# Optimization experiments

Measured on AMD Instinct MI355X. Metric: run time of the kernel, lower is better.

## Reference

```python
import jax, jax.numpy as jnp
import numpy as np

INPUT_DIM, HIDDEN_DIM, N_HEADS, N_AGENTS = 256, 512, 8, 64
BATCH, N_ENTITIES = 128, 256


def setup_inputs() -> dict:
    key = jax.random.key(0)
    ks = jax.random.split(key, 6)
    x = jax.random.normal(ks[0], (BATCH, N_ENTITIES, INPUT_DIM), dtype=jnp.float32)
    # encode: LeakyReLU -> Linear(input_dim, hidden_dim)
    W_enc = jax.random.normal(ks[1], (INPUT_DIM, HIDDEN_DIM), dtype=jnp.float32) * (1.0 / np.sqrt(INPUT_DIM))
    b_enc = jnp.zeros((HIDDEN_DIM,), dtype=jnp.float32)
    # per-head full hidden x hidden projections, stacked on head axis
    WQ = jax.random.normal(ks[2], (N_HEADS, HIDDEN_DIM, HIDDEN_DIM), dtype=jnp.float32)
    WK = jax.random.normal(ks[3], (N_HEADS, HIDDEN_DIM, HIDDEN_DIM), dtype=jnp.float32)
    WV = jax.random.normal(ks[4], (N_HEADS, HIDDEN_DIM, HIDDEN_DIM), dtype=jnp.float32)
    return {"x": x, "W_enc": W_enc, "b_enc": b_enc, "WQ": WQ, "WK": WK, "WV": WV, "n_agents": N_AGENTS}


def reference(x, W_enc, b_enc, WQ, WK, WV, n_agents):
    scale = 1.0 / np.sqrt(WQ.shape[-1]).astype(np.float32)
    # encode: LeakyReLU(0.01) then Linear
    h = jax.nn.leaky_relu(x, negative_slope=0.01) @ W_enc + b_enc  # [b, e, H]
    ha = h[:, :n_agents]  # [b, a, H]
    # all heads at once: n = head axis
    Q = jnp.einsum('bah,nhd->nbad', ha, WQ)
    K = jnp.einsum('beh,nhd->nbed', h, WK)
    V = jnp.einsum('beh,nhd->nbed', h, WV)
    scores = jnp.einsum('nbad,nbed->nbae', Q, K) * scale
    p = jax.nn.softmax(scores, axis=-1)
    # redundant renormalization from the original code
    prob = p / (jnp.sum(p, axis=-1, keepdims=True) + 1e-12)
    z = jnp.einsum('nbae,nbed->nbad', prob, V)  # [n, b, a, H]
    return jnp.mean(z, axis=0)  # [b, a, H]
```

## Files before the change

kernel.cpp:

```cpp
#include <hip/hip_runtime.h>
#include <math.h>

#define BATCH  128
#define NENT   256
#define INDIM  256
#define HID    512
#define NHEAD  8
#define NAGENT 64
#define SCALE  0.04419417382415922f

typedef unsigned short u16;
typedef unsigned int   u32;

typedef __bf16 bf16x8  __attribute__((ext_vector_type(8)));
typedef float  floatx4 __attribute__((ext_vector_type(4)));
typedef u32    u32x4   __attribute__((ext_vector_type(4)));
typedef u32    u32x2   __attribute__((ext_vector_type(2)));

union Frag {
    u32x4 s;
    struct { u32x2 lo, hi; } p;
    bf16x8 v;
};

__device__ __forceinline__ u16 f2bf(float x) {
    u32 u = __float_as_uint(x);
    return (u16)((u + 0x7FFFu + ((u >> 16) & 1u)) >> 16);
}
__device__ __forceinline__ float bf2f(u16 b) {
    return __uint_as_float(((u32)b) << 16);
}
__device__ __forceinline__ void split4(const float4& r, ushort4& hh, ushort4& hl) {
    hh.x = f2bf(r.x); hl.x = f2bf(r.x - bf2f(hh.x));
    hh.y = f2bf(r.y); hl.y = f2bf(r.y - bf2f(hh.y));
    hh.z = f2bf(r.z); hl.z = f2bf(r.z - bf2f(hh.z));
    hh.w = f2bf(r.w); hl.w = f2bf(r.w - bf2f(hh.w));
}

__global__ __launch_bounds__(256) void wenc_t_kernel(const float* __restrict__ W,
                                                     u16* __restrict__ Wt_h,
                                                     u16* __restrict__ Wt_l) {
    __shared__ float tile[64][68];
    const int bid = blockIdx.x;
    const int k0 = (bid & 3) * 64;
    const int d0 = (bid >> 2) * 64;
    const int t = threadIdx.x;
    const int ki = t >> 2, dc = (t & 3) * 16;
    #pragma unroll
    for (int c = 0; c < 4; ++c)
        *(float4*)&tile[ki][dc + c * 4] =
            *(const float4*)(W + (size_t)(k0 + ki) * HID + d0 + dc + c * 4);
    __syncthreads();
    const int dr = t >> 2, kc = (t & 3) * 16;
    #pragma unroll
    for (int c = 0; c < 4; ++c) {
        float4 v = make_float4(tile[kc + c * 4 + 0][dr], tile[kc + c * 4 + 1][dr],
                               tile[kc + c * 4 + 2][dr], tile[kc + c * 4 + 3][dr]);
        ushort4 hh, hl; split4(v, hh, hl);
        size_t o = (size_t)(d0 + dr) * INDIM + k0 + kc + c * 4;
        *(ushort4*)(Wt_h + o) = hh;
        *(ushort4*)(Wt_l + o) = hl;
    }
}

__global__ __launch_bounds__(256) void enc_kernel(const float* __restrict__ x,
                                                  const u16* __restrict__ Wt_h,
                                                  const u16* __restrict__ Wt_l,
                                                  const float* __restrict__ bias,
                                                  u16* __restrict__ h_h,
                                                  u16* __restrict__ h_l) {
    __shared__ u16 Ah[32][264];
    __shared__ u16 Al[32][264];
    const int r0 = blockIdx.x * 32;
    const int t  = threadIdx.x;
    {
        const int row = t >> 3;
        const float* xr = x + (size_t)(r0 + row) * INDIM;
        #pragma unroll
        for (int j = 0; j < 8; ++j) {
            const int k0 = ((t & 7) + j * 8) * 4;
            float4 v = *(const float4*)(xr + k0);
            v.x = v.x > 0.f ? v.x : 0.01f * v.x;
            v.y = v.y > 0.f ? v.y : 0.01f * v.y;
            v.z = v.z > 0.f ? v.z : 0.01f * v.z;
            v.w = v.w > 0.f ? v.w : 0.01f * v.w;
            ushort4 hh, hl; split4(v, hh, hl);
            *(ushort4*)&Ah[row][k0] = hh;
            *(ushort4*)&Al[row][k0] = hl;
        }
    }
    __syncthreads();

    const int wid = t >> 6, lane = t & 63, l15 = lane & 15, quad = lane >> 4;
    const int mbase = (wid & 1) * 16;
    const int nbase = (wid >> 1) * 256;
    const floatx4 z4 = {0.f, 0.f, 0.f, 0.f};
    floatx4 acc[16];
    #pragma unroll
    for (int i = 0; i < 16; ++i) acc[i] = z4;

    for (int ks = 0; ks < 8; ++ks) {
        const int k = ks * 32 + quad * 8;
        Frag Afh, Afl;
        Afh.s = *(const u32x4*)&Ah[mbase + l15][k];
        Afl.s = *(const u32x4*)&Al[mbase + l15][k];
        #pragma unroll
        for (int nt = 0; nt < 16; ++nt) {
            const int d = nbase + nt * 16 + l15;
            Frag Bh, Bl;
            Bh.s = *(const u32x4*)(Wt_h + (size_t)d * INDIM + k);
            Bl.s = *(const u32x4*)(Wt_l + (size_t)d * INDIM + k);
            floatx4 c = acc[nt];
            c = __builtin_amdgcn_mfma_f32_16x16x32_bf16(Afh.v, Bh.v, c, 0, 0, 0);
            c = __builtin_amdgcn_mfma_f32_16x16x32_bf16(Afh.v, Bl.v, c, 0, 0, 0);
            c = __builtin_amdgcn_mfma_f32_16x16x32_bf16(Afl.v, Bh.v, c, 0, 0, 0);
            acc[nt] = c;
        }
    }
    #pragma unroll
    for (int nt = 0; nt < 16; ++nt) {
        const int d = nbase + nt * 16 + l15;
        const float bv = bias[d];
        #pragma unroll
        for (int r = 0; r < 4; ++r) {
            const float v = acc[nt][r] + bv;
            const u16 hi = f2bf(v);
            const u16 lo = f2bf(v - bf2f(hi));
            const size_t o = (size_t)(r0 + mbase + quad * 4 + r) * HID + d;
            h_h[o] = hi;
            h_l[o] = lo;
        }
    }
}

__global__ __launch_bounds__(256) void ht_kernel(const u16* __restrict__ h_h,
                                                 u16* __restrict__ hT) {
    __shared__ u16 tile[64][72];
    const int bid = blockIdx.x;
    const int dt = bid & 7;
    const int et = (bid >> 3) & 3;
    const int b  = bid >> 5;
    const int t  = threadIdx.x;
    const int r  = t >> 2, cs = (t & 3) * 16;
    const u16* src = h_h + (size_t)(b * 256 + et * 64 + r) * HID + dt * 64 + cs;
    *(ushort4*)&tile[r][cs + 0]  = *(const ushort4*)(src + 0);
    *(ushort4*)&tile[r][cs + 4]  = *(const ushort4*)(src + 4);
    *(ushort4*)&tile[r][cs + 8]  = *(const ushort4*)(src + 8);
    *(ushort4*)&tile[r][cs + 12] = *(const ushort4*)(src + 12);
    __syncthreads();
    const int d = t >> 2, es = (t & 3) * 16;
    u16* dst = hT + (size_t)b * 131072 + (size_t)(dt * 64 + d) * 256 + et * 64 + es;
    #pragma unroll
    for (int c = 0; c < 4; ++c) {
        ushort4 v = make_ushort4(tile[es + c * 4 + 0][d], tile[es + c * 4 + 1][d],
                                 tile[es + c * 4 + 2][d], tile[es + c * 4 + 3][d]);
        *(ushort4*)(dst + c * 4) = v;
    }
}

__global__ __launch_bounds__(256) void wqk_kernel(const float* __restrict__ WQ,
                                                  const float* __restrict__ WK,
                                                  u16* __restrict__ Mt_h,
                                                  u16* __restrict__ Mt_l) {
    __shared__ u16 Ah[64][72], Al[64][72], Bh[64][72], Bl[64][72];
    const int bid = blockIdx.x;
    const int jt = (bid & 7) * 64;
    const int it = ((bid >> 3) & 7) * 64;
    const int n  = bid >> 6;
    const float* qp = WQ + (size_t)n * 262144;
    const float* kp = WK + (size_t)n * 262144;
    const int t = threadIdx.x;
    const int wid = t >> 6, lane = t & 63, l15 = lane & 15, quad = lane >> 4;
    const int srow = t >> 2, sc = (t & 3) * 16;

    const floatx4 z4 = {0.f, 0.f, 0.f, 0.f};
    floatx4 acc[4];
    #pragma unroll
    for (int i = 0; i < 4; ++i) acc[i] = z4;

    for (int kc = 0; kc < HID; kc += 64) {
        #pragma unroll
        for (int f = 0; f < 4; ++f) {
            float4 va = *(const float4*)(kp + (size_t)(jt + srow) * HID + kc + sc + f * 4);
            ushort4 hh, hl; split4(va, hh, hl);
            *(ushort4*)&Ah[srow][sc + f * 4] = hh;
            *(ushort4*)&Al[srow][sc + f * 4] = hl;
            float4 vb = *(const float4*)(qp + (size_t)(it + srow) * HID + kc + sc + f * 4);
            split4(vb, hh, hl);
            *(ushort4*)&Bh[srow][sc + f * 4] = hh;
            *(ushort4*)&Bl[srow][sc + f * 4] = hl;
        }
        __syncthreads();
        #pragma unroll
        for (int ks = 0; ks < 2; ++ks) {
            const int k = ks * 32 + quad * 8;
            Frag Afh, Afl;
            Afh.s = *(const u32x4*)&Ah[wid * 16 + l15][k];
            Afl.s = *(const u32x4*)&Al[wid * 16 + l15][k];
            #pragma unroll
            for (int nt = 0; nt < 4; ++nt) {
                Frag Bfh, Bfl;
                Bfh.s = *(const u32x4*)&Bh[nt * 16 + l15][k];
                Bfl.s = *(const u32x4*)&Bl[nt * 16 + l15][k];
                floatx4 c = acc[nt];
                c = __builtin_amdgcn_mfma_f32_16x16x32_bf16(Afh.v, Bfh.v, c, 0, 0, 0);
                c = __builtin_amdgcn_mfma_f32_16x16x32_bf16(Afh.v, Bfl.v, c, 0, 0, 0);
                c = __builtin_amdgcn_mfma_f32_16x16x32_bf16(Afl.v, Bfh.v, c, 0, 0, 0);
                acc[nt] = c;
            }
        }
        __syncthreads();
    }
    #pragma unroll
    for (int nt = 0; nt < 4; ++nt)
        #pragma unroll
        for (int r = 0; r < 4; ++r) {
            const float v = acc[nt][r] * SCALE;
            const u16 hi = f2bf(v);
            const u16 lo = f2bf(v - bf2f(hi));
            const int j = jt + wid * 16 + quad * 4 + r;
            const int i = it + nt * 16 + l15;
            const size_t o = (size_t)n * 262144 + (size_t)j * HID + i;
            Mt_h[o] = hi;
            Mt_l[o] = lo;
        }
}

__global__ __launch_bounds__(256) void wvt_kernel(const float* __restrict__ WV,
                                                  u16* __restrict__ WVt) {
    __shared__ float tile[64][68];
    const int bid = blockIdx.x;
    const int i0 = (bid & 7) * 64;
    const int o0 = ((bid >> 3) & 7) * 64;
    const int n  = bid >> 6;
    const float* src = WV + (size_t)n * 262144;
    const int t  = threadIdx.x;
    const int di = t >> 2;
    const int dc = (t & 3) * 16;
    #pragma unroll
    for (int c = 0; c < 4; ++c)
        *(float4*)&tile[di][dc + c * 4] =
            *(const float4*)(src + (size_t)(i0 + di) * HID + o0 + dc + c * 4);
    __syncthreads();
    const int dr = t >> 2;
    const int ic = (t & 3) * 16;
    size_t o = (size_t)n * 262144 + (size_t)(o0 + dr) * HID + i0 + ic;
    #pragma unroll
    for (int c = 0; c < 4; ++c) {
        ushort4 v = make_ushort4(f2bf(tile[ic + c * 4 + 0][dr]), f2bf(tile[ic + c * 4 + 1][dr]),
                                 f2bf(tile[ic + c * 4 + 2][dr]), f2bf(tile[ic + c * 4 + 3][dr]));
        *(ushort4*)(WVt + o + c * 4) = v;
    }
}

template<bool USE_HT>
__global__ __launch_bounds__(256, 3) void attn_kernel(const u16* __restrict__ h_h,
                                                      const u16* __restrict__ h_l,
                                                      const u16* __restrict__ Mt_h,
                                                      const u16* __restrict__ Mt_l,
                                                      const u16* __restrict__ WVt,
                                                      const u16* __restrict__ hT,
                                                      float* __restrict__ out) {
    __shared__ __align__(16) char SM[53504];
    u16*   Th  = (u16*)SM;
    u16*   Tl  = (u16*)(SM + 16640);
    float* S   = (float*)SM;
    float* red = (float*)(SM + 33792);
    u16*   HbT = (u16*)SM;
    u16*   U   = (u16*)SM;
    u16*   Pt  = (u16*)(SM + 36864);

    const int bid = blockIdx.x;
    const int x7 = bid & 7;
    const int s  = bid >> 3;
    const int at = s & 1;
    const int n  = (x7 >> 1) | (((s >> 1) & 1) << 2);
    const int b  = ((s >> 2) << 1) | (x7 & 1);

    const int tid  = threadIdx.x;
    const int wid  = tid >> 6;
    const int lane = tid & 63;
    const int l15  = lane & 15;
    const int quad = lane >> 4;

    const u16* Mth = Mt_h + (size_t)n * 262144;
    const u16* Mtl = Mt_l + (size_t)n * 262144;
    const u16* Wv  = WVt  + (size_t)n * 262144;
    const u16* hTb = hT + (size_t)b * 131072;
    const size_t hb_base = (size_t)b * NENT * HID;
    const size_t ha_base = hb_base + (size_t)at * 32 * HID;

    const floatx4 z4 = {0.f, 0.f, 0.f, 0.f};
    floatx4 Sacc[8];
    #pragma unroll
    for (int i = 0; i < 8; ++i) Sacc[i] = z4;

    for (int H = 0; H < 2; ++H) {
        floatx4 Tacc[8];
        #pragma unroll
        for (int i = 0; i < 8; ++i) Tacc[i] = z4;
        Frag Bh[2][4], Bl[2][4];
        auto loadBA = [&](int ksv, Frag* bh, Frag* bl) {
            const int k = ksv * 32 + quad * 8;
            #pragma unroll
            for (int nt = 0; nt < 4; ++nt) {
                const int d = H * 256 + (wid * 4 + nt) * 16 + l15;
                bh[nt].s = *(const u32x4*)(Mth + (size_t)d * HID + k);
                bl[nt].s = *(const u32x4*)(Mtl + (size_t)d * HID + k);
            }
        };
        loadBA(0, Bh[0], Bl[0]);
        #pragma unroll 2
        for (int ks = 0; ks < 16; ++ks) {
            const int cur = ks & 1, nxt = cur ^ 1;
            const int k = ks * 32 + quad * 8;
            Frag Ahf[2], Alf[2];
            #pragma unroll
            for (int mt = 0; mt < 2; ++mt) {
                const size_t ro = ha_base + (size_t)(mt * 16 + l15) * HID + k;
                Ahf[mt].s = *(const u32x4*)(h_h + ro);
                Alf[mt].s = *(const u32x4*)(h_l + ro);
            }
            if (ks < 15) loadBA(ks + 1, Bh[nxt], Bl[nxt]);
            #pragma unroll
            for (int nt = 0; nt < 4; ++nt)
                #pragma unroll
                for (int mt = 0; mt < 2; ++mt) {
                    floatx4 c = Tacc[mt * 4 + nt];
                    c = __builtin_amdgcn_mfma_f32_16x16x32_bf16(Ahf[mt].v, Bh[cur][nt].v, c, 0, 0, 0);
                    c = __builtin_amdgcn_mfma_f32_16x16x32_bf16(Ahf[mt].v, Bl[cur][nt].v, c, 0, 0, 0);
                    c = __builtin_amdgcn_mfma_f32_16x16x32_bf16(Alf[mt].v, Bh[cur][nt].v, c, 0, 0, 0);
                    Tacc[mt * 4 + nt] = c;
                }
        }
        __syncthreads();
        #pragma unroll
        for (int mt = 0; mt < 2; ++mt)
            #pragma unroll
            for (int nt = 0; nt < 4; ++nt)
                #pragma unroll
                for (int r = 0; r < 4; ++r) {
                    const float v = Tacc[mt * 4 + nt][r];
                    const int a  = mt * 16 + quad * 4 + r;
                    const int dl = (wid * 4 + nt) * 16 + l15;
                    const u16 hi = f2bf(v);
                    Th[a * 260 + dl] = hi;
                    Tl[a * 260 + dl] = f2bf(v - bf2f(hi));
                }
        __syncthreads();
        Frag Ahb[2][4], Alb[2][4];
        auto loadAB2 = [&](int ksv, Frag* ah, Frag* al) {
            const int kg = H * 256 + ksv * 32 + quad * 8;
            #pragma unroll
            for (int mt = 0; mt < 4; ++mt) {
                const size_t ro = hb_base + (size_t)((wid * 4 + mt) * 16 + l15) * HID + kg;
                ah[mt].s = *(const u32x4*)(h_h + ro);
                al[mt].s = *(const u32x4*)(h_l + ro);
            }
        };
        loadAB2(0, Ahb[0], Alb[0]);
        #pragma unroll 2
        for (int ks = 0; ks < 8; ++ks) {
            const int cur = ks & 1, nxt = cur ^ 1;
            const int kl = ks * 32 + quad * 8;
            if (ks < 7) loadAB2(ks + 1, Ahb[nxt], Alb[nxt]);
            #pragma unroll
            for (int nt = 0; nt < 2; ++nt) {
                const int ac = nt * 16 + l15;
                Frag Bfh, Bfl;
                Bfh.p.lo = *(const u32x2*)(Th + ac * 260 + kl);
                Bfh.p.hi = *(const u32x2*)(Th + ac * 260 + kl + 4);
                Bfl.p.lo = *(const u32x2*)(Tl + ac * 260 + kl);
                Bfl.p.hi = *(const u32x2*)(Tl + ac * 260 + kl + 4);
                #pragma unroll
                for (int mt = 0; mt < 4; ++mt) {
                    floatx4 c = Sacc[mt * 2 + nt];
                    c = __builtin_amdgcn_mfma_f32_16x16x32_bf16(Ahb[cur][mt].v, Bfh.v, c, 0, 0, 0);
                    c = __builtin_amdgcn_mfma_f32_16x16x32_bf16(Ahb[cur][mt].v, Bfl.v, c, 0, 0, 0);
                    c = __builtin_amdgcn_mfma_f32_16x16x32_bf16(Alb[cur][mt].v, Bfh.v, c, 0, 0, 0);
                    Sacc[mt * 2 + nt] = c;
                }
            }
        }
    }
    __syncthreads();
    #pragma unroll
    for (int mt = 0; mt < 4; ++mt)
        #pragma unroll
        for (int nt = 0; nt < 2; ++nt)
            #pragma unroll
            for (int r = 0; r < 4; ++r) {
                const int e = (wid * 4 + mt) * 16 + quad * 4 + r;
                const int a = nt * 16 + l15;
                S[e * 33 + a] = Sacc[mt * 2 + nt][r];
            }
    __syncthreads();
    {
        const int a   = tid & 31;
        const int seg = tid >> 5;
        float v[32];
        #pragma unroll
        for (int i = 0; i < 32; ++i) v[i] = S[(seg * 32 + i) * 33 + a];
        float mx = v[0];
        #pragma unroll
        for (int i = 1; i < 32; ++i) mx = fmaxf(mx, v[i]);
        red[a * 8 + seg] = mx;
        __syncthreads();
        float gmx = red[a * 8 + 0];
        #pragma unroll
        for (int i = 1; i < 8; ++i) gmx = fmaxf(gmx, red[a * 8 + i]);
        __syncthreads();
        float sum = 0.f;
        #pragma unroll
        for (int i = 0; i < 32; ++i) { v[i] = expf(v[i] - gmx); sum += v[i]; }
        red[a * 8 + seg] = sum;
        __syncthreads();
        float tot = 0.f;
        #pragma unroll
        for (int i = 0; i < 8; ++i) tot += red[a * 8 + i];
        const float inv = 1.0f / tot;
        #pragma unroll
        for (int i = 0; i < 32; ++i)
            Pt[a * 260 + seg * 32 + i] = f2bf(v[i] * inv);
    }
    __syncthreads();
    floatx4 Uacc[16];
    #pragma unroll
    for (int i = 0; i < 16; ++i) Uacc[i] = z4;
    const int d0w = wid * 128;
    if (USE_HT) {
        Frag Bc[2][8];
        auto loadBC = [&](int etv, Frag* bc) {
            #pragma unroll
            for (int dt = 0; dt < 8; ++dt) {
                const int d = d0w + dt * 16 + l15;
                bc[dt].s = *(const u32x4*)(hTb + (size_t)d * 256 + etv * 32 + quad * 8);
            }
        };
        loadBC(0, Bc[0]);
        #pragma unroll 2
        for (int et = 0; et < 8; ++et) {
            const int cur = et & 1, nxt = cur ^ 1;
            if (et < 7) loadBC(et + 1, Bc[nxt]);
            Frag Ap[2];
            #pragma unroll
            for (int mt = 0; mt < 2; ++mt) {
                const int ar = mt * 16 + l15;
                Ap[mt].p.lo = *(const u32x2*)(Pt + ar * 260 + et * 32 + quad * 8);
                Ap[mt].p.hi = *(const u32x2*)(Pt + ar * 260 + et * 32 + quad * 8 + 4);
            }
            #pragma unroll
            for (int dt = 0; dt < 8; ++dt)
                #pragma unroll
                for (int mt = 0; mt < 2; ++mt)
                    Uacc[mt * 8 + dt] = __builtin_amdgcn_mfma_f32_16x16x32_bf16(Ap[mt].v, Bc[cur][dt].v, Uacc[mt * 8 + dt], 0, 0, 0);
        }
    } else {
        u32* Hb32 = (u32*)HbT;
        for (int et = 0; et < 8; ++et) {
            {
                const int ep = lane & 15;
                const int q  = lane >> 4;
                const size_t r0 = hb_base + (size_t)(et * 32 + 2 * ep) * HID;
                #pragma unroll
                for (int c = 0; c < 4; ++c) {
                    const int d0 = d0w + c * 32 + q * 8;
                    u32x4 u0 = *(const u32x4*)(h_h + r0 + d0);
                    u32x4 u1 = *(const u32x4*)(h_h + r0 + HID + d0);
                    #pragma unroll
                    for (int p = 0; p < 4; ++p) {
                        const u32 w0 = (u0[p] & 0xFFFFu) | (u1[p] << 16);
                        const u32 w1 = (u0[p] >> 16) | (u1[p] & 0xFFFF0000u);
                        Hb32[(d0 + 2 * p) * 18 + ep]     = w0;
                        Hb32[(d0 + 2 * p + 1) * 18 + ep] = w1;
                    }
                }
            }
            Frag Ap[2];
            #pragma unroll
            for (int mt = 0; mt < 2; ++mt) {
                const int ar = mt * 16 + l15;
                Ap[mt].p.lo = *(const u32x2*)(Pt + ar * 260 + et * 32 + quad * 8);
                Ap[mt].p.hi = *(const u32x2*)(Pt + ar * 260 + et * 32 + quad * 8 + 4);
            }
            #pragma unroll
            for (int dt = 0; dt < 8; ++dt) {
                const int d = d0w + dt * 16 + l15;
                Frag Bf;
                Bf.p.lo = *(const u32x2*)(HbT + d * 36 + quad * 8);
                Bf.p.hi = *(const u32x2*)(HbT + d * 36 + quad * 8 + 4);
                #pragma unroll
                for (int mt = 0; mt < 2; ++mt)
                    Uacc[mt * 8 + dt] = __builtin_amdgcn_mfma_f32_16x16x32_bf16(Ap[mt].v, Bf.v, Uacc[mt * 8 + dt], 0, 0, 0);
            }
        }
    }
    __syncthreads();
    #pragma unroll
    for (int mt = 0; mt < 2; ++mt)
        #pragma unroll
        for (int dt = 0; dt < 8; ++dt)
            #pragma unroll
            for (int r = 0; r < 4; ++r) {
                const int a = mt * 16 + quad * 4 + r;
                const int d = d0w + dt * 16 + l15;
                U[a * 520 + d] = f2bf(Uacc[mt * 8 + dt][r]);
            }
    __syncthreads();
    floatx4 Zacc[16];
    #pragma unroll
    for (int i = 0; i < 16; ++i) Zacc[i] = z4;
    Frag Bw[2][8];
    auto loadBD = [&](int ksv, Frag* bw) {
        const int k = ksv * 32 + quad * 8;
        #pragma unroll
        for (int dt = 0; dt < 8; ++dt) {
            const int dn = (wid * 8 + dt) * 16 + l15;
            bw[dt].s = *(const u32x4*)(Wv + (size_t)dn * HID + k);
        }
    };
    loadBD(0, Bw[0]);
    #pragma unroll 2
    for (int ks = 0; ks < 16; ++ks) {
        const int cur = ks & 1, nxt = cur ^ 1;
        const int k = ks * 32 + quad * 8;
        Frag Au[2];
        #pragma unroll
        for (int mt = 0; mt < 2; ++mt) {
            Au[mt].p.lo = *(const u32x2*)(U + (mt * 16 + l15) * 520 + k);
            Au[mt].p.hi = *(const u32x2*)(U + (mt * 16 + l15) * 520 + k + 4);
        }
        if (ks < 15) loadBD(ks + 1, Bw[nxt]);
        #pragma unroll
        for (int dt = 0; dt < 8; ++dt)
            #pragma unroll
            for (int mt = 0; mt < 2; ++mt)
                Zacc[mt * 8 + dt] = __builtin_amdgcn_mfma_f32_16x16x32_bf16(Au[mt].v, Bw[cur][dt].v, Zacc[mt * 8 + dt], 0, 0, 0);
    }
    float* ob = out + ((size_t)b * NAGENT + at * 32) * HID;
    #pragma unroll
    for (int mt = 0; mt < 2; ++mt)
        #pragma unroll
        for (int dt = 0; dt < 8; ++dt)
            #pragma unroll
            for (int r = 0; r < 4; ++r) {
                const int a  = mt * 16 + quad * 4 + r;
                const int dn = (wid * 8 + dt) * 16 + l15;
                atomicAdd(ob + (size_t)a * HID + dn, Zacc[mt * 8 + dt][r] * 0.125f);
            }
}

extern "C" void kernel_launch(void* const* d_in, const int* in_sizes, int n_in,
                              void* d_out, int out_size, void* d_ws, size_t ws_size,
                              hipStream_t stream) {
    const float* x     = (const float*)d_in[0];
    const float* W_enc = (const float*)d_in[1];
    const float* b_enc = (const float*)d_in[2];
    const float* WQ    = (const float*)d_in[3];
    const float* WK    = (const float*)d_in[4];
    const float* WV    = (const float*)d_in[5];
    float* out = (float*)d_out;

    char* ws = (char*)d_ws;
    u16* h_h  = (u16*)ws;
    u16* h_l  = (u16*)(ws + 33554432);
    u16* Mt_h = (u16*)(ws + 67108864);
    u16* Mt_l = (u16*)(ws + 71303168);
    u16* WVt  = (u16*)(ws + 75497472);
    u16* hT   = (u16*)(ws + 79691776);
    u16* Wt_h = WVt;
    u16* Wt_l = WVt + 131072;

    const bool useHT = ws_size >= (size_t)113246208;

    hipMemsetAsync(d_out, 0, (size_t)out_size * sizeof(float), stream);
    wenc_t_kernel<<<32, 256, 0, stream>>>(W_enc, Wt_h, Wt_l);
    enc_kernel<<<1024, 256, 0, stream>>>(x, Wt_h, Wt_l, b_enc, h_h, h_l);
    if (useHT) ht_kernel<<<4096, 256, 0, stream>>>(h_h, hT);
    wvt_kernel<<<512, 256, 0, stream>>>(WV, WVt);
    wqk_kernel<<<512, 256, 0, stream>>>(WQ, WK, Mt_h, Mt_l);
    if (useHT)
        attn_kernel<true><<<2048, 256, 0, stream>>>(h_h, h_l, Mt_h, Mt_l, WVt, hT, out);
    else
        attn_kernel<false><<<2048, 256, 0, stream>>>(h_h, h_l, Mt_h, Mt_l, WVt, hT, out);
}
```

Baseline: 989.2 us.

## Interleave bf16 hi/lo split planes into packed layout and drop register double-buffering

Stores the hi and lo bf16 halves of h, the QK product matrix, and the encoder weight interleaved in 32-element chunks within one buffer. A fragment's hi and lo parts then sit 64 bytes apart in the same cache lines rather than in two separate arrays. Several GEMM loops also lose their explicit next-step register prefetch and instead load fragments per step or per pair of steps, which lowers register pressure but exposes more load latency. Every producer and consumer kernel is updated to the new indexing.

```diff
diff --git a/kernel.cpp b/kernel.cpp
--- a/kernel.cpp
+++ b/kernel.cpp
@@ -9,6 +9,7 @@
 #define NAGENT 64
 #define SCALE  0.04419417382415922f
 
+
 typedef unsigned short u16;
 typedef unsigned int   u32;
 
@@ -38,8 +39,7 @@
 }
 
 __global__ __launch_bounds__(256) void wenc_t_kernel(const float* __restrict__ W,
-                                                     u16* __restrict__ Wt_h,
-                                                     u16* __restrict__ Wt_l) {
+                                                     u16* __restrict__ Wt_p) {
     __shared__ float tile[64][68];
     const int bid = blockIdx.x;
     const int k0 = (bid & 3) * 64;
@@ -57,18 +57,17 @@
         float4 v = make_float4(tile[kc + c * 4 + 0][dr], tile[kc + c * 4 + 1][dr],
                                tile[kc + c * 4 + 2][dr], tile[kc + c * 4 + 3][dr]);
         ushort4 hh, hl; split4(v, hh, hl);
-        size_t o = (size_t)(d0 + dr) * INDIM + k0 + kc + c * 4;
-        *(ushort4*)(Wt_h + o) = hh;
-        *(ushort4*)(Wt_l + o) = hl;
+        const int kk = k0 + kc + c * 4;
+        size_t o = (size_t)(d0 + dr) * 512 + (size_t)(kk >> 5) * 64 + (kk & 31);
+        *(ushort4*)(Wt_p + o) = hh;
+        *(ushort4*)(Wt_p + o + 32) = hl;
     }
 }
 
 __global__ __launch_bounds__(256) void enc_kernel(const float* __restrict__ x,
-                                                  const u16* __restrict__ Wt_h,
-                                                  const u16* __restrict__ Wt_l,
+                                                  const u16* __restrict__ Wt_p,
                                                   const float* __restrict__ bias,
-                                                  u16* __restrict__ h_h,
-                                                  u16* __restrict__ h_l) {
+                                                  u16* __restrict__ h_p) {
     __shared__ u16 Ah[32][264];
     __shared__ u16 Al[32][264];
     const int r0 = blockIdx.x * 32;
@@ -107,9 +106,10 @@
         #pragma unroll
         for (int nt = 0; nt < 16; ++nt) {
             const int d = nbase + nt * 16 + l15;
+            const size_t wo = (size_t)d * 512 + (size_t)ks * 64 + quad * 8;
             Frag Bh, Bl;
-            Bh.s = *(const u32x4*)(Wt_h + (size_t)d * INDIM + k);
-            Bl.s = *(const u32x4*)(Wt_l + (size_t)d * INDIM + k);
+            Bh.s = *(const u32x4*)(Wt_p + wo);
+            Bl.s = *(const u32x4*)(Wt_p + wo + 32);
             floatx4 c = acc[nt];
             c = __builtin_amdgcn_mfma_f32_16x16x32_bf16(Afh.v, Bh.v, c, 0, 0, 0);
             c = __builtin_amdgcn_mfma_f32_16x16x32_bf16(Afh.v, Bl.v, c, 0, 0, 0);
@@ -126,14 +126,15 @@
             const float v = acc[nt][r] + bv;
             const u16 hi = f2bf(v);
             const u16 lo = f2bf(v - bf2f(hi));
-            const size_t o = (size_t)(r0 + mbase + quad * 4 + r) * HID + d;
-            h_h[o] = hi;
-            h_l[o] = lo;
-        }
-    }
-}
-
-__global__ __launch_bounds__(256) void ht_kernel(const u16* __restrict__ h_h,
+            const size_t o = (size_t)(r0 + mbase + quad * 4 + r) * 1024
+                           + (size_t)(d >> 5) * 64 + (d & 31);
+            h_p[o]      = hi;
+            h_p[o + 32] = lo;
+        }
+    }
+}
+
+__global__ __launch_bounds__(256) void ht_kernel(const u16* __restrict__ h_p,
                                                  u16* __restrict__ hT) {
     __shared__ u16 tile[64][72];
     const int bid = blockIdx.x;
@@ -142,7 +143,9 @@
     const int b  = bid >> 5;
     const int t  = threadIdx.x;
     const int r  = t >> 2, cs = (t & 3) * 16;
-    const u16* src = h_h + (size_t)(b * 256 + et * 64 + r) * HID + dt * 64 + cs;
+    const int dg = dt * 64 + cs;
+    const u16* src = h_p + (size_t)(b * 256 + et * 64 + r) * 1024
+                   + (size_t)(dg >> 5) * 64 + (dg & 31);
     *(ushort4*)&tile[r][cs + 0]  = *(const ushort4*)(src + 0);
     *(ushort4*)&tile[r][cs + 4]  = *(const ushort4*)(src + 4);
     *(ushort4*)&tile[r][cs + 8]  = *(const ushort4*)(src + 8);
@@ -160,8 +163,7 @@
 
 __global__ __launch_bounds__(256) void wqk_kernel(const float* __restrict__ WQ,
                                                   const float* __restrict__ WK,
-                                                  u16* __restrict__ Mt_h,
-                                                  u16* __restrict__ Mt_l) {
+                                                  u16* __restrict__ Mt_p) {
     __shared__ u16 Ah[64][72], Al[64][72], Bh[64][72], Bl[64][72];
     const int bid = blockIdx.x;
     const int jt = (bid & 7) * 64;
@@ -220,9 +222,10 @@
             const u16 lo = f2bf(v - bf2f(hi));
             const int j = jt + wid * 16 + quad * 4 + r;
             const int i = it + nt * 16 + l15;
-            const size_t o = (size_t)n * 262144 + (size_t)j * HID + i;
-            Mt_h[o] = hi;
-            Mt_l[o] = lo;
+            const size_t o = (size_t)n * 524288 + (size_t)j * 1024
+                           + (size_t)(i >> 5) * 64 + (i & 31);
+            Mt_p[o]      = hi;
+            Mt_p[o + 32] = lo;
         }
 }
 
@@ -254,10 +257,8 @@
 }
 
 template<bool USE_HT>
-__global__ __launch_bounds__(256, 3) void attn_kernel(const u16* __restrict__ h_h,
-                                                      const u16* __restrict__ h_l,
-                                                      const u16* __restrict__ Mt_h,
-                                                      const u16* __restrict__ Mt_l,
+__global__ __launch_bounds__(256, 3) void attn_kernel(const u16* __restrict__ h_p,
+                                                      const u16* __restrict__ Mt_p,
                                                       const u16* __restrict__ WVt,
                                                       const u16* __restrict__ hT,
                                                       float* __restrict__ out) {
@@ -283,12 +284,11 @@
     const int l15  = lane & 15;
     const int quad = lane >> 4;
 
-    const u16* Mth = Mt_h + (size_t)n * 262144;
-    const u16* Mtl = Mt_l + (size_t)n * 262144;
+    const u16* Mtp = Mt_p + (size_t)n * 524288;
     const u16* Wv  = WVt  + (size_t)n * 262144;
     const u16* hTb = hT + (size_t)b * 131072;
-    const size_t hb_base = (size_t)b * NENT * HID;
-    const size_t ha_base = hb_base + (size_t)at * 32 * HID;
+    const size_t hb_base = (size_t)b * 262144;
+    const size_t ha_row0 = hb_base + (size_t)(at * 32) * 1024;
 
     const floatx4 z4 = {0.f, 0.f, 0.f, 0.f};
     floatx4 Sacc[8];
@@ -299,39 +299,31 @@
         floatx4 Tacc[8];
         #pragma unroll
         for (int i = 0; i < 8; ++i) Tacc[i] = z4;
-        Frag Bh[2][4], Bl[2][4];
-        auto loadBA = [&](int ksv, Frag* bh, Frag* bl) {
-            const int k = ksv * 32 + quad * 8;
+        for (int ks = 0; ks < 16; ++ks) {
+            const int ko = ks * 64 + quad * 8;
+            Frag Ahf[2], Alf[2];
+            #pragma unroll
+            for (int mt = 0; mt < 2; ++mt) {
+                const size_t ro = ha_row0 + (size_t)(mt * 16 + l15) * 1024 + ko;
+                Ahf[mt].s = *(const u32x4*)(h_p + ro);
+                Alf[mt].s = *(const u32x4*)(h_p + ro + 32);
+            }
             #pragma unroll
             for (int nt = 0; nt < 4; ++nt) {
                 const int d = H * 256 + (wid * 4 + nt) * 16 + l15;
-                bh[nt].s = *(const u32x4*)(Mth + (size_t)d * HID + k);
-                bl[nt].s = *(const u32x4*)(Mtl + (size_t)d * HID + k);
-            }
-        };
-        loadBA(0, Bh[0], Bl[0]);
-        #pragma unroll 2
-        for (int ks = 0; ks < 16; ++ks) {
-            const int cur = ks & 1, nxt = cur ^ 1;
-            const int k = ks * 32 + quad * 8;
-            Frag Ahf[2], Alf[2];
-            #pragma unroll
-            for (int mt = 0; mt < 2; ++mt) {
-                const size_t ro = ha_base + (size_t)(mt * 16 + l15) * HID + k;
-                Ahf[mt].s = *(const u32x4*)(h_h + ro);
-                Alf[mt].s = *(const u32x4*)(h_l + ro);
-            }
-            if (ks < 15) loadBA(ks + 1, Bh[nxt], Bl[nxt]);
-            #pragma unroll
-            for (int nt = 0; nt < 4; ++nt)
+                const size_t mo = (size_t)d * 1024 + ko;
+                Frag Bh, Bl;
+                Bh.s = *(const u32x4*)(Mtp + mo);
+                Bl.s = *(const u32x4*)(Mtp + mo + 32);
                 #pragma unroll
                 for (int mt = 0; mt < 2; ++mt) {
                     floatx4 c = Tacc[mt * 4 + nt];
-                    c = __builtin_amdgcn_mfma_f32_16x16x32_bf16(Ahf[mt].v, Bh[cur][nt].v, c, 0, 0, 0);
-                    c = __builtin_amdgcn_mfma_f32_16x16x32_bf16(Ahf[mt].v, Bl[cur][nt].v, c, 0, 0, 0);
-                    c = __builtin_amdgcn_mfma_f32_16x16x32_bf16(Alf[mt].v, Bh[cur][nt].v, c, 0, 0, 0);
+                    c = __builtin_amdgcn_mfma_f32_16x16x32_bf16(Ahf[mt].v, Bh.v, c, 0, 0, 0);
+                    c = __builtin_amdgcn_mfma_f32_16x16x32_bf16(Ahf[mt].v, Bl.v, c, 0, 0, 0);
+                    c = __builtin_amdgcn_mfma_f32_16x16x32_bf16(Alf[mt].v, Bh.v, c, 0, 0, 0);
                     Tacc[mt * 4 + nt] = c;
                 }
+            }
         }
         __syncthreads();
         #pragma unroll
@@ -348,22 +340,16 @@
                     Tl[a * 260 + dl] = f2bf(v - bf2f(hi));
                 }
         __syncthreads();
-        Frag Ahb[2][4], Alb[2][4];
-        auto loadAB2 = [&](int ksv, Frag* ah, Frag* al) {
-            const int kg = H * 256 + ksv * 32 + quad * 8;
+        for (int ks = 0; ks < 8; ++ks) {
+            const int kl = ks * 32 + quad * 8;
+            const int ko = (H * 8 + ks) * 64 + quad * 8;
+            Frag Ahf[4], Alf[4];
             #pragma unroll
             for (int mt = 0; mt < 4; ++mt) {
-                const size_t ro = hb_base + (size_t)((wid * 4 + mt) * 16 + l15) * HID + kg;
-                ah[mt].s = *(const u32x4*)(h_h + ro);
-                al[mt].s = *(const u32x4*)(h_l + ro);
-            }
-        };
-        loadAB2(0, Ahb[0], Alb[0]);
-        #pragma unroll 2
-        for (int ks = 0; ks < 8; ++ks) {
-            const int cur = ks & 1, nxt = cur ^ 1;
-            const int kl = ks * 32 + quad * 8;
-            if (ks < 7) loadAB2(ks + 1, Ahb[nxt], Alb[nxt]);
+                const size_t ro = hb_base + (size_t)((wid * 4 + mt) * 16 + l15) * 1024 + ko;
+                Ahf[mt].s = *(const u32x4*)(h_p + ro);
+                Alf[mt].s = *(const u32x4*)(h_p + ro + 32);
+            }
             #pragma unroll
             for (int nt = 0; nt < 2; ++nt) {
                 const int ac = nt * 16 + l15;
@@ -375,9 +361,9 @@
                 #pragma unroll
                 for (int mt = 0; mt < 4; ++mt) {
                     floatx4 c = Sacc[mt * 2 + nt];
-                    c = __builtin_amdgcn_mfma_f32_16x16x32_bf16(Ahb[cur][mt].v, Bfh.v, c, 0, 0, 0);
-                    c = __builtin_amdgcn_mfma_f32_16x16x32_bf16(Ahb[cur][mt].v, Bfl.v, c, 0, 0, 0);
-                    c = __builtin_amdgcn_mfma_f32_16x16x32_bf16(Alb[cur][mt].v, Bfh.v, c, 0, 0, 0);
+                    c = __builtin_amdgcn_mfma_f32_16x16x32_bf16(Ahf[mt].v, Bfh.v, c, 0, 0, 0);
+                    c = __builtin_amdgcn_mfma_f32_16x16x32_bf16(Ahf[mt].v, Bfl.v, c, 0, 0, 0);
+                    c = __builtin_amdgcn_mfma_f32_16x16x32_bf16(Alf[mt].v, Bfh.v, c, 0, 0, 0);
                     Sacc[mt * 2 + nt] = c;
                 }
             }
@@ -429,50 +415,53 @@
     for (int i = 0; i < 16; ++i) Uacc[i] = z4;
     const int d0w = wid * 128;
     if (USE_HT) {
-        Frag Bc[2][8];
-        auto loadBC = [&](int etv, Frag* bc) {
-            #pragma unroll
-            for (int dt = 0; dt < 8; ++dt) {
-                const int d = d0w + dt * 16 + l15;
-                bc[dt].s = *(const u32x4*)(hTb + (size_t)d * 256 + etv * 32 + quad * 8);
-            }
-        };
-        loadBC(0, Bc[0]);
-        #pragma unroll 2
-        for (int et = 0; et < 8; ++et) {
-            const int cur = et & 1, nxt = cur ^ 1;
-            if (et < 7) loadBC(et + 1, Bc[nxt]);
-            Frag Ap[2];
-            #pragma unroll
-            for (int mt = 0; mt < 2; ++mt) {
-                const int ar = mt * 16 + l15;
-                Ap[mt].p.lo = *(const u32x2*)(Pt + ar * 260 + et * 32 + quad * 8);
-                Ap[mt].p.hi = *(const u32x2*)(Pt + ar * 260 + et * 32 + quad * 8 + 4);
-            }
-            #pragma unroll
-            for (int dt = 0; dt < 8; ++dt)
-                #pragma unroll
-                for (int mt = 0; mt < 2; ++mt)
-                    Uacc[mt * 8 + dt] = __builtin_amdgcn_mfma_f32_16x16x32_bf16(Ap[mt].v, Bc[cur][dt].v, Uacc[mt * 8 + dt], 0, 0, 0);
+        for (int ep = 0; ep < 4; ++ep) {
+            Frag Bc[2][8];
+            #pragma unroll
+            for (int sb = 0; sb < 2; ++sb)
+                #pragma unroll
+                for (int dt = 0; dt < 8; ++dt) {
+                    const int d = d0w + dt * 16 + l15;
+                    Bc[sb][dt].s = *(const u32x4*)(hTb + (size_t)d * 256
+                                                   + (2 * ep + sb) * 32 + quad * 8);
+                }
+            #pragma unroll
+            for (int sb = 0; sb < 2; ++sb) {
+                const int et = 2 * ep + sb;
+                Frag Ap[2];
+                #pragma unroll
+                for (int mt = 0; mt < 2; ++mt) {
+                    const int ar = mt * 16 + l15;
+                    Ap[mt].p.lo = *(const u32x2*)(Pt + ar * 260 + et * 32 + quad * 8);
+                    Ap[mt].p.hi = *(const u32x2*)(Pt + ar * 260 + et * 32 + quad * 8 + 4);
+                }
+                #pragma unroll
+                for (int dt = 0; dt < 8; ++dt)
+                    #pragma unroll
+                    for (int mt = 0; mt < 2; ++mt)
+                        Uacc[mt * 8 + dt] = __builtin_amdgcn_mfma_f32_16x16x32_bf16(
+                            Ap[mt].v, Bc[sb][dt].v, Uacc[mt * 8 + dt], 0, 0, 0);
+            }
         }
     } else {
         u32* Hb32 = (u32*)HbT;
         for (int et = 0; et < 8; ++et) {
             {
-                const int ep = lane & 15;
-                const int q  = lane >> 4;
-                const size_t r0 = hb_base + (size_t)(et * 32 + 2 * ep) * HID;
+                const int epi = lane & 15;
+                const int q   = lane >> 4;
+                const size_t r0p = hb_base + (size_t)(et * 32 + 2 * epi) * 1024;
                 #pragma unroll
                 for (int c = 0; c < 4; ++c) {
                     const int d0 = d0w + c * 32 + q * 8;
-                    u32x4 u0 = *(const u32x4*)(h_h + r0 + d0);
-                    u32x4 u1 = *(const u32x4*)(h_h + r0 + HID + d0);
+                    const size_t po = (size_t)(d0 >> 5) * 64 + (d0 & 31);
+                    u32x4 u0 = *(const u32x4*)(h_p + r0p + po);
+                    u32x4 u1 = *(const u32x4*)(h_p + r0p + 1024 + po);
                     #pragma unroll
                     for (int p = 0; p < 4; ++p) {
                         const u32 w0 = (u0[p] & 0xFFFFu) | (u1[p] << 16);
                         const u32 w1 = (u0[p] >> 16) | (u1[p] & 0xFFFF0000u);
-                        Hb32[(d0 + 2 * p) * 18 + ep]     = w0;
-                        Hb32[(d0 + 2 * p + 1) * 18 + ep] = w1;
+                        Hb32[(d0 + 2 * p) * 18 + epi]     = w0;
+                        Hb32[(d0 + 2 * p + 1) * 18 + epi] = w1;
                     }
                 }
             }
@@ -491,7 +480,8 @@
                 Bf.p.hi = *(const u32x2*)(HbT + d * 36 + quad * 8 + 4);
                 #pragma unroll
                 for (int mt = 0; mt < 2; ++mt)
-                    Uacc[mt * 8 + dt] = __builtin_amdgcn_mfma_f32_16x16x32_bf16(Ap[mt].v, Bf.v, Uacc[mt * 8 + dt], 0, 0, 0);
+                    Uacc[mt * 8 + dt] = __builtin_amdgcn_mfma_f32_16x16x32_bf16(
+                        Ap[mt].v, Bf.v, Uacc[mt * 8 + dt], 0, 0, 0);
             }
         }
     }
@@ -510,32 +500,33 @@
     floatx4 Zacc[16];
     #pragma unroll
     for (int i = 0; i < 16; ++i) Zacc[i] = z4;
-    Frag Bw[2][8];
-    auto loadBD = [&](int ksv, Frag* bw) {
-        const int k = ksv * 32 + quad * 8;
-        #pragma unroll
-        for (int dt = 0; dt < 8; ++dt) {
-            const int dn = (wid * 8 + dt) * 16 + l15;
-            bw[dt].s = *(const u32x4*)(Wv + (size_t)dn * HID + k);
-        }
-    };
-    loadBD(0, Bw[0]);
-    #pragma unroll 2
-    for (int ks = 0; ks < 16; ++ks) {
-        const int cur = ks & 1, nxt = cur ^ 1;
-        const int k = ks * 32 + quad * 8;
-        Frag Au[2];
-        #pragma unroll
-        for (int mt = 0; mt < 2; ++mt) {
-            Au[mt].p.lo = *(const u32x2*)(U + (mt * 16 + l15) * 520 + k);
-            Au[mt].p.hi = *(const u32x2*)(U + (mt * 16 + l15) * 520 + k + 4);
-        }
-        if (ks < 15) loadBD(ks + 1, Bw[nxt]);
-        #pragma unroll
-        for (int dt = 0; dt < 8; ++dt)
-            #pragma unroll
-            for (int mt = 0; mt < 2; ++mt)
-                Zacc[mt * 8 + dt] = __builtin_amdgcn_mfma_f32_16x16x32_bf16(Au[mt].v, Bw[cur][dt].v, Zacc[mt * 8 + dt], 0, 0, 0);
+    for (int kp = 0; kp < 8; ++kp) {
+        Frag Bw[2][8];
+        #pragma unroll
+        for (int sb = 0; sb < 2; ++sb) {
+            const int k = (kp * 2 + sb) * 32 + quad * 8;
+            #pragma unroll
+            for (int dt = 0; dt < 8; ++dt) {
+                const int dn = (wid * 8 + dt) * 16 + l15;
+                Bw[sb][dt].s = *(const u32x4*)(Wv + (size_t)dn * HID + k);
+            }
+        }
+        #pragma unroll
+        for (int sb = 0; sb < 2; ++sb) {
+            const int k = (kp * 2 + sb) * 32 + quad * 8;
+            Frag Au[2];
+            #pragma unroll
+            for (int mt = 0; mt < 2; ++mt) {
+                Au[mt].p.lo = *(const u32x2*)(U + (mt * 16 + l15) * 520 + k);
+                Au[mt].p.hi = *(const u32x2*)(U + (mt * 16 + l15) * 520 + k + 4);
+            }
+            #pragma unroll
+            for (int dt = 0; dt < 8; ++dt)
+                #pragma unroll
+                for (int mt = 0; mt < 2; ++mt)
+                    Zacc[mt * 8 + dt] = __builtin_amdgcn_mfma_f32_16x16x32_bf16(
+                        Au[mt].v, Bw[sb][dt].v, Zacc[mt * 8 + dt], 0, 0, 0);
+        }
     }
     float* ob = out + ((size_t)b * NAGENT + at * 32) * HID;
     #pragma unroll
@@ -562,25 +553,22 @@
     float* out = (float*)d_out;
 
     char* ws = (char*)d_ws;
-    u16* h_h  = (u16*)ws;
-    u16* h_l  = (u16*)(ws + 33554432);
-    u16* Mt_h = (u16*)(ws + 67108864);
-    u16* Mt_l = (u16*)(ws + 71303168);
+    u16* h_p  = (u16*)ws;
+    u16* Mt_p = (u16*)(ws + 67108864);
     u16* WVt  = (u16*)(ws + 75497472);
     u16* hT   = (u16*)(ws + 79691776);
-    u16* Wt_h = WVt;
-    u16* Wt_l = WVt + 131072;
+    u16* Wt_p = WVt;
 
     const bool useHT = ws_size >= (size_t)113246208;
 
     hipMemsetAsync(d_out, 0, (size_t)out_size * sizeof(float), stream);
-    wenc_t_kernel<<<32, 256, 0, stream>>>(W_enc, Wt_h, Wt_l);
-    enc_kernel<<<1024, 256, 0, stream>>>(x, Wt_h, Wt_l, b_enc, h_h, h_l);
-    if (useHT) ht_kernel<<<4096, 256, 0, stream>>>(h_h, hT);
+    wenc_t_kernel<<<32, 256, 0, stream>>>(W_enc, Wt_p);
+    enc_kernel<<<1024, 256, 0, stream>>>(x, Wt_p, b_enc, h_p);
+    if (useHT) ht_kernel<<<4096, 256, 0, stream>>>(h_p, hT);
     wvt_kernel<<<512, 256, 0, stream>>>(WV, WVt);
-    wqk_kernel<<<512, 256, 0, stream>>>(WQ, WK, Mt_h, Mt_l);
+    wqk_kernel<<<512, 256, 0, stream>>>(WQ, WK, Mt_p);
     if (useHT)
-        attn_kernel<true><<<2048, 256, 0, stream>>>(h_h, h_l, Mt_h, Mt_l, WVt, hT, out);
+        attn_kernel<true><<<2048, 256, 0, stream>>>(h_p, Mt_p, WVt, hT, out);
     else
-        attn_kernel<false><<<2048, 256, 0, stream>>>(h_h, h_l, Mt_h, Mt_l, WVt, hT, out);
-}
+        attn_kernel<false><<<2048, 256, 0, stream>>>(h_p, Mt_p, WVt, hT, out);
+}
```

Result: faster. 967.1 us (-2.2%).
